# Optimization experiments

Hardware: AMD Instinct MI355X
Metric: run time of the kernel (lower is better)

The kernel has to match this reference:

```python
import jax, jax.numpy as jnp
import numpy as np

B, C, H, W = 8, 320, 32, 32
HEADS, DHEAD = 8, 40
CTX_LEN, CTX_DIM = 77, 768
FF_INNER = 4 * C
GROUPS = 32
HW = H * W


def setup_inputs() -> dict:
    key = jax.random.key(0)
    ks = jax.random.split(key, 16)
    def nrm(k, shape, s=0.02):
        return (jax.random.normal(k, shape) * s).astype(jnp.float32)
    z = lambda *s: jnp.zeros(s, jnp.float32)
    o = lambda *s: jnp.ones(s, jnp.float32)
    inp = {}
    inp["x"] = jax.random.normal(ks[0], (B, C, H, W), jnp.float32)
    inp["context"] = jax.random.normal(ks[1], (B, CTX_LEN, CTX_DIM), jnp.float32)
    inp["vis_mask"] = jax.random.uniform(ks[2], (B, HW, HW)) > 0.5
    inp["v2t_mask"] = jax.random.uniform(ks[3], (B, HW, CTX_LEN)) > 0.5
    inp["gn_scale"] = o(C); inp["gn_bias"] = z(C)
    inp["proj_in_w"] = nrm(ks[4], (C, C)); inp["proj_in_b"] = z(C)
    inp["n1_s"] = o(C); inp["n1_b"] = z(C)
    inp["wq1"] = nrm(ks[5], (C, C)); inp["wk1"] = nrm(ks[6], (C, C)); inp["wv1"] = nrm(ks[7], (C, C))
    inp["wo1"] = nrm(ks[8], (C, C)); inp["bo1"] = z(C)
    inp["n2_s"] = o(C); inp["n2_b"] = z(C)
    inp["wq2"] = nrm(ks[9], (C, C)); inp["wk2"] = nrm(ks[10], (CTX_DIM, C)); inp["wv2"] = nrm(ks[11], (CTX_DIM, C))
    inp["wo2"] = nrm(ks[12], (C, C)); inp["bo2"] = z(C)
    inp["n3_s"] = o(C); inp["n3_b"] = z(C)
    inp["ff_w1"] = nrm(ks[13], (C, 2 * FF_INNER)); inp["ff_b1"] = z(2 * FF_INNER)
    inp["ff_w2"] = nrm(ks[14], (FF_INNER, C)); inp["ff_b2"] = z(C)
    inp["proj_out_w"] = nrm(ks[15], (C, C)); inp["proj_out_b"] = z(C)
    return inp


def group_norm(x, scale, bias, eps=1e-6):
    b, c, h, w = x.shape
    xg = x.reshape(b, GROUPS, -1)
    mu = xg.mean(-1, keepdims=True)
    var = xg.var(-1, keepdims=True)
    xn = ((xg - mu) * jax.lax.rsqrt(var + eps)).reshape(b, c, h, w)
    return xn * scale[None, :, None, None] + bias[None, :, None, None]


def layer_norm(x, s, b, eps=1e-5):
    mu = x.mean(-1, keepdims=True)
    var = x.var(-1, keepdims=True)
    return (x - mu) * jax.lax.rsqrt(var + eps) * s + b


def mha(xq, ctx, wq, wk, wv, wo, bo, mask):
    # CrossAttention: manual einsum softmax with boolean mask broadcast over heads
    b, n, _ = xq.shape
    m = ctx.shape[1]
    split = lambda t: t.reshape(b, -1, HEADS, DHEAD).transpose(0, 2, 1, 3)
    q = split(xq @ wq)   # [b,h,n,d]
    k = split(ctx @ wk)  # [b,h,m,d]
    v = split(ctx @ wv)
    sim = jnp.einsum('bhid,bhjd->bhij', q, k) * (DHEAD ** -0.5)
    if mask is not None:
        sim = jnp.where(mask[:, None, :, :], sim, jnp.finfo(sim.dtype).min)
    attn = jax.nn.softmax(sim, axis=-1)
    out = jnp.einsum('bhij,bhjd->bhid', attn, v)
    out = out.transpose(0, 2, 1, 3).reshape(b, n, HEADS * DHEAD)
    return out @ wo + bo


def reference(x, context, vis_mask, v2t_mask, gn_scale, gn_bias, proj_in_w, proj_in_b,
              n1_s, n1_b, wq1, wk1, wv1, wo1, bo1,
              n2_s, n2_b, wq2, wk2, wv2, wo2, bo2,
              n3_s, n3_b, ff_w1, ff_b1, ff_w2, ff_b2,
              proj_out_w, proj_out_b):
    x_in = x
    h = group_norm(x, gn_scale, gn_bias)
    # 1x1 conv proj_in == per-pixel linear; flatten b c h w -> b (hw) c
    h = h.reshape(B, C, HW).transpose(0, 2, 1) @ proj_in_w + proj_in_b
    # masked self-attention (vis mask)
    h = h + mha(layer_norm(h, n1_s, n1_b), layer_norm(h, n1_s, n1_b),
                wq1, wk1, wv1, wo1, bo1, vis_mask)
    # masked cross-attention to text (v2t mask)
    h = h + mha(layer_norm(h, n2_s, n2_b), context,
                wq2, wk2, wv2, wo2, bo2, v2t_mask)
    # GEGLU feedforward (glu=True, mult=4)
    y = layer_norm(h, n3_s, n3_b) @ ff_w1 + ff_b1
    a, g = jnp.split(y, 2, axis=-1)
    h = h + (a * jax.nn.gelu(g, approximate=False)) @ ff_w2 + ff_b2
    # proj_out + residual
    out = (h @ proj_out_w + proj_out_b).transpose(0, 2, 1).reshape(B, C, H, W)
    return out + x_in
```

## Files before the change

### kernel.cpp

```cpp
#include <hip/hip_runtime.h>
#include <hip/hip_bf16.h>
#include <math.h>


#define Bsz   8
#define Cch   320
#define HW    1024
#define NTOK  (Bsz*HW)
#define HEADS 8
#define DHEAD 40
#define CTXL  77
#define CTXD  768
#define FFI   1280
#define MCTX  (Bsz*CTXL)
#define MCTXP 640

typedef unsigned short u16;
typedef unsigned long long u64;
typedef __attribute__((ext_vector_type(8))) u16    u16x8;
typedef __attribute__((ext_vector_type(8))) __bf16 bf16x8;
typedef __attribute__((ext_vector_type(4))) float  f32x4;

__device__ inline u16 f2b(float f) {
    unsigned u = __float_as_uint(f);
    return (u16)((u + 0x7FFFu + ((u >> 16) & 1u)) >> 16);
}

__global__ __launch_bounds__(256) void gn_stats(
    const float* __restrict__ x, const float* __restrict__ scale,
    const float* __restrict__ bias, float* __restrict__ gnA,
    float* __restrict__ gnB)
{
    int blk = blockIdx.x;
    int b = blk >> 5, g = blk & 31;
    int tid = threadIdx.x;
    __shared__ float rs[256], rq[256];
    const float4* xg = (const float4*)(x + ((size_t)b*Cch + g*10)*HW);
    float s = 0.f, q = 0.f;
    #pragma unroll
    for (int i = 0; i < 10; ++i) {
        float4 v = xg[tid + i*256];
        s += v.x + v.y + v.z + v.w;
        q += v.x*v.x + v.y*v.y + v.z*v.z + v.w*v.w;
    }
    rs[tid] = s; rq[tid] = q; __syncthreads();
    for (int off = 128; off > 0; off >>= 1) {
        if (tid < off) { rs[tid] += rs[tid+off]; rq[tid] += rq[tid+off]; }
        __syncthreads();
    }
    if (tid < 10) {
        float mean = rs[0] * (1.f/10240.f);
        float var  = rq[0] * (1.f/10240.f) - mean*mean;
        float inv  = rsqrtf(var + 1e-6f);
        int ch = g*10 + tid;
        float a = inv * scale[ch];
        gnA[b*Cch + ch] = a;
        gnB[b*Cch + ch] = bias[ch] - mean*a;
    }
}

__global__ __launch_bounds__(256) void gn_apply(
    const float* __restrict__ x, const float* __restrict__ gnA,
    const float* __restrict__ gnB, u16* __restrict__ out)
{
    __shared__ u16 T[64*72];
    const int tid = threadIdx.x;
    const int c0 = blockIdx.x * 64;
    const int p0 = blockIdx.y * 64;
    const int b  = blockIdx.z;
    for (int e = tid; e < 512; e += 256) {
        int r = e >> 3, ch = e & 7;
        const float* src = x + ((size_t)(b*Cch + c0 + r))*HW + p0 + ch*8;
        float a  = gnA[b*Cch + c0 + r];
        float bb = gnB[b*Cch + c0 + r];
        float4 v0 = *(const float4*)src;
        float4 v1 = *(const float4*)(src + 4);
        u16x8 val;
        val[0] = f2b(v0.x*a + bb); val[1] = f2b(v0.y*a + bb);
        val[2] = f2b(v0.z*a + bb); val[3] = f2b(v0.w*a + bb);
        val[4] = f2b(v1.x*a + bb); val[5] = f2b(v1.y*a + bb);
        val[6] = f2b(v1.z*a + bb); val[7] = f2b(v1.w*a + bb);
// ... 26 lines not shown
        sum += __shfl_xor(sum, off);
        sq  += __shfl_xor(sq,  off);
    }
    float mean = sum * (1.f/320.f);
    float var  = sq  * (1.f/320.f) - mean*mean;
    float inv  = rsqrtf(var + 1e-5f);
    u16* orow = out + (size_t)t*Cch;
    #pragma unroll
    for (int i = 0; i < 5; ++i) {
        int c = lane + 64*i;
        orow[c] = f2b((v[i]-mean)*inv*s[c] + bgain[c]);
    }
}

struct WDesc { const float* src; u16* dst; int K; int N; int tiles; float scl; };
struct WPack { WDesc w[12]; };

#define WT_TILES 620
#define CTXBLK   240

__global__ __launch_bounds__(256) void preamble(
    WPack p, const float* __restrict__ ctxsrc, u16* __restrict__ ctxdst,
    const void* __restrict__ vis, const void* __restrict__ v2t,
    u64* __restrict__ bvis, u64* __restrict__ bv2t)
{
    __shared__ u16 T[64*72];
    int blk = blockIdx.x;
    int tid = threadIdx.x;
    if (blk < WT_TILES) {
        int t = blk;
        #pragma unroll
        for (int i = 0; i < 12; ++i) {
            int nt = p.w[i].tiles;
            if (t < nt) {
                const int K = p.w[i].K, N = p.w[i].N;
                const int ntN = N >> 6;
                const int tk = t / ntN, tn = t - tk*ntN;
                const float scl = p.w[i].scl;
                const float* src = p.w[i].src;
                u16* dst = p.w[i].dst;
                for (int e = tid; e < 512; e += 256) {
                    int r = e >> 3, ch = e & 7;
                    const float* sp = src + (size_t)(tk*64 + r)*N + tn*64 + ch*8;
                    float4 v0 = *(const float4*)sp;
                    float4 v1 = *(const float4*)(sp + 4);
                    u16x8 val;
                    val[0] = f2b(v0.x*scl); val[1] = f2b(v0.y*scl);
// ... 9 lines not shown
                    dst[(size_t)(tn*64 + n)*K + tk*64 + k] = v;
                }
                return;
            }
            t -= nt;
        }
        return;
    }
    if (blk < WT_TILES + CTXBLK) {
        int idx = (blk - WT_TILES)*2048 + tid*8;
        int r = idx / CTXD;
        u16x8 val = {};
        if (r < MCTX) {
            float4 v0 = *(const float4*)(ctxsrc + idx);
            float4 v1 = *(const float4*)(ctxsrc + idx + 4);
            val[0] = f2b(v0.x); val[1] = f2b(v0.y);
            val[2] = f2b(v0.z); val[3] = f2b(v0.w);
            val[4] = f2b(v1.x); val[5] = f2b(v1.y);
            val[6] = f2b(v1.z); val[7] = f2b(v1.w);
        }
        *(u16x8*)(ctxdst + idx) = val;
        return;
    }
    __shared__ int any;
    if (tid == 0) any = 0;
    __syncthreads();
    const unsigned char* probe = (const unsigned char*)vis;
    for (int i = tid; i < 4096; i += 256)
        if ((i & 3) && probe[i]) any = 1;
    __syncthreads();
    const int isU8 = any;
    int mb = blk - WT_TILES - CTXBLK;
    const void* mask; u64* bits; int Lkv, nw;
    if (mb < 2048) { mask = vis; bits = bvis; Lkv = HW;   nw = 16; }
    else           { mask = v2t; bits = bv2t; Lkv = CTXL; nw = 2; mb -= 2048; }
    const int wv = tid >> 6, lane = tid & 63;
    const int row = mb*4 + wv;
    const unsigned char* m8  = (const unsigned char*)mask;
    const int*           m32 = (const int*)mask;
    const size_t base = (size_t)row * Lkv;
    for (int w = 0; w < nw; ++w) {
        int j = w*64 + lane;
        bool on = (j < Lkv) && (isU8 ? (m8[base+j] != 0) : (m32[base+j] != 0));
        u64 word = __ballot(on);
        if (lane == 0) bits[(size_t)row*nw + w] = word;
    }
}

__global__ __launch_bounds__(256) void gemm_bf16(
    const u16* __restrict__ A, const u16* __restrict__ Wt,
    const float* __restrict__ bias, const float* __restrict__ res,
    float* __restrict__ out, u16* __restrict__ out_bf, int M, int N, int K)
{
    __shared__ u16 As[2][128*40];
    __shared__ u16 Bs[2][64*40];
    const int tid  = threadIdx.x;
    const int lane = tid & 63;
    const int w    = tid >> 6;
    const int m0   = blockIdx.y * 128;
    const int n0   = blockIdx.x * 64;
    const int fr   = lane & 15, fg = lane >> 4;
    const int ar   = tid >> 2, ac = tid & 3;

    const u16* pa0 = A  + (size_t)(m0 + ar)*K      + ac*8;
    const u16* pa1 = A  + (size_t)(m0 + ar + 64)*K + ac*8;
    const u16* pb  = Wt + (size_t)(n0 + ar)*K      + ac*8;
    const int nk = K >> 5;

    *(u16x8*)&As[0][ar*40 + ac*8]      = *(const u16x8*)pa0;
    *(u16x8*)&As[0][(ar+64)*40 + ac*8] = *(const u16x8*)pa1;
    *(u16x8*)&Bs[0][ar*40 + ac*8]      = *(const u16x8*)pb;
    u16x8 xa0 = *(const u16x8*)(pa0 + 32);
    u16x8 xa1 = *(const u16x8*)(pa1 + 32);
    u16x8 xb  = *(const u16x8*)(pb  + 32);
    u16x8 ya0 = *(const u16x8*)(pa0 + 64);
    u16x8 ya1 = *(const u16x8*)(pa1 + 64);
    u16x8 yb  = *(const u16x8*)(pb  + 64);

    f32x4 acc[2][4] = {};
    for (int i = 0; i < nk; i += 2) {
        __syncthreads();
        *(u16x8*)&As[1][ar*40 + ac*8]      = xa0;
        *(u16x8*)&As[1][(ar+64)*40 + ac*8] = xa1;
        *(u16x8*)&Bs[1][ar*40 + ac*8]      = xb;
        if (i + 3 < nk) {
            xa0 = *(const u16x8*)(pa0 + 32*(i+3));
            xa1 = *(const u16x8*)(pa1 + 32*(i+3));
            xb  = *(const u16x8*)(pb  + 32*(i+3));
        }
        {
            bf16x8 a0 = *(const bf16x8*)&As[0][(w*32      + fr)*40 + fg*8];
            bf16x8 a1 = *(const bf16x8*)&As[0][(w*32 + 16 + fr)*40 + fg*8];
            #pragma unroll
            for (int nt = 0; nt < 4; ++nt) {
                bf16x8 b = *(const bf16x8*)&Bs[0][(nt*16 + fr)*40 + fg*8];
                acc[0][nt] = __builtin_amdgcn_mfma_f32_16x16x32_bf16(a0, b, acc[0][nt], 0, 0, 0);
                acc[1][nt] = __builtin_amdgcn_mfma_f32_16x16x32_bf16(a1, b, acc[1][nt], 0, 0, 0);
            }
        }
        __syncthreads();
        if (i + 2 < nk) {
            *(u16x8*)&As[0][ar*40 + ac*8]      = ya0;
            *(u16x8*)&As[0][(ar+64)*40 + ac*8] = ya1;
            *(u16x8*)&Bs[0][ar*40 + ac*8]      = yb;
            if (i + 4 < nk) {
                ya0 = *(const u16x8*)(pa0 + 32*(i+4));
                ya1 = *(const u16x8*)(pa1 + 32*(i+4));
                yb  = *(const u16x8*)(pb  + 32*(i+4));
            }
        }
        {
            bf16x8 a0 = *(const bf16x8*)&As[1][(w*32      + fr)*40 + fg*8];
            bf16x8 a1 = *(const bf16x8*)&As[1][(w*32 + 16 + fr)*40 + fg*8];
            #pragma unroll
            for (int nt = 0; nt < 4; ++nt) {
                bf16x8 b = *(const bf16x8*)&Bs[1][(nt*16 + fr)*40 + fg*8];
                acc[0][nt] = __builtin_amdgcn_mfma_f32_16x16x32_bf16(a0, b, acc[0][nt], 0, 0, 0);
                acc[1][nt] = __builtin_amdgcn_mfma_f32_16x16x32_bf16(a1, b, acc[1][nt], 0, 0, 0);
            }
        }
    }
    #pragma unroll
    for (int at = 0; at < 2; ++at) {
        #pragma unroll
        for (int nt = 0; nt < 4; ++nt) {
            int gn = n0 + nt*16 + fr;
            float bv = bias ? bias[gn] : 0.f;
            #pragma unroll
            for (int i = 0; i < 4; ++i) {
                int gm = m0 + w*32 + at*16 + fg*4 + i;
                float v = acc[at][nt][i] + bv;
                if (res) v += res[(size_t)gm*N + gn];
                if (out) out[(size_t)gm*N + gn] = v;
                if (out_bf) out_bf[(size_t)gm*N + gn] = f2b(v);
            }
        }
    }
}

__global__ __launch_bounds__(256) void gemm_pout(
    const u16* __restrict__ A, const u16* __restrict__ Wt,
    const float* __restrict__ bias, const float* __restrict__ x,
    float* __restrict__ out, int K)
{
    __shared__ u16 As[2][128*40];
    __shared__ u16 Bs[2][64*40];
    const int tid  = threadIdx.x;
    const int lane = tid & 63;
    const int w    = tid >> 6;
    const int m0   = blockIdx.y * 128;
    const int n0   = blockIdx.x * 64;
    const int fr   = lane & 15, fg = lane >> 4;
    const int ar   = tid >> 2, ac = tid & 3;

    const u16* pa0 = A  + (size_t)(m0 + ar)*K      + ac*8;
    const u16* pa1 = A  + (size_t)(m0 + ar + 64)*K + ac*8;
    const u16* pb  = Wt + (size_t)(n0 + ar)*K      + ac*8;
    const int nk = K >> 5;

    *(u16x8*)&As[0][ar*40 + ac*8]      = *(const u16x8*)pa0;
    *(u16x8*)&As[0][(ar+64)*40 + ac*8] = *(const u16x8*)pa1;
    *(u16x8*)&Bs[0][ar*40 + ac*8]      = *(const u16x8*)pb;
    u16x8 xa0 = *(const u16x8*)(pa0 + 32);
    u16x8 xa1 = *(const u16x8*)(pa1 + 32);
    u16x8 xb  = *(const u16x8*)(pb  + 32);
    u16x8 ya0 = *(const u16x8*)(pa0 + 64);
    u16x8 ya1 = *(const u16x8*)(pa1 + 64);
    u16x8 yb  = *(const u16x8*)(pb  + 64);

    f32x4 acc[2][4] = {};
    for (int i = 0; i < nk; i += 2) {
        __syncthreads();
        *(u16x8*)&As[1][ar*40 + ac*8]      = xa0;
        *(u16x8*)&As[1][(ar+64)*40 + ac*8] = xa1;
        *(u16x8*)&Bs[1][ar*40 + ac*8]      = xb;
        if (i + 3 < nk) {
            xa0 = *(const u16x8*)(pa0 + 32*(i+3));
            xa1 = *(const u16x8*)(pa1 + 32*(i+3));
            xb  = *(const u16x8*)(pb  + 32*(i+3));
        }
        {
            bf16x8 a0 = *(const bf16x8*)&As[0][(w*32      + fr)*40 + fg*8];
            bf16x8 a1 = *(const bf16x8*)&As[0][(w*32 + 16 + fr)*40 + fg*8];
            #pragma unroll
            for (int nt = 0; nt < 4; ++nt) {
                bf16x8 b = *(const bf16x8*)&Bs[0][(nt*16 + fr)*40 + fg*8];
                acc[0][nt] = __builtin_amdgcn_mfma_f32_16x16x32_bf16(a0, b, acc[0][nt], 0, 0, 0);
                acc[1][nt] = __builtin_amdgcn_mfma_f32_16x16x32_bf16(a1, b, acc[1][nt], 0, 0, 0);
            }
        }
        __syncthreads();
        if (i + 2 < nk) {
            *(u16x8*)&As[0][ar*40 + ac*8]      = ya0;
            *(u16x8*)&As[0][(ar+64)*40 + ac*8] = ya1;
            *(u16x8*)&Bs[0][ar*40 + ac*8]      = yb;
            if (i + 4 < nk) {
                ya0 = *(const u16x8*)(pa0 + 32*(i+4));
                ya1 = *(const u16x8*)(pa1 + 32*(i+4));
                yb  = *(const u16x8*)(pb  + 32*(i+4));
            }
        }
        {
            bf16x8 a0 = *(const bf16x8*)&As[1][(w*32      + fr)*40 + fg*8];
            bf16x8 a1 = *(const bf16x8*)&As[1][(w*32 + 16 + fr)*40 + fg*8];
            #pragma unroll
            for (int nt = 0; nt < 4; ++nt) {
                bf16x8 b = *(const bf16x8*)&Bs[1][(nt*16 + fr)*40 + fg*8];
                acc[0][nt] = __builtin_amdgcn_mfma_f32_16x16x32_bf16(a0, b, acc[0][nt], 0, 0, 0);
                acc[1][nt] = __builtin_amdgcn_mfma_f32_16x16x32_bf16(a1, b, acc[1][nt], 0, 0, 0);
            }
        }
    }
    #pragma unroll
    for (int at = 0; at < 2; ++at) {
        #pragma unroll
        for (int nt = 0; nt < 4; ++nt) {
            int gn = n0 + nt*16 + fr;
            float bv = bias[gn];
            int gm0 = m0 + w*32 + at*16 + fg*4;
            int b   = gm0 >> 10;
            int p   = gm0 & (HW-1);
            size_t o = ((size_t)(b*Cch + gn))*HW + p;
            f32x4 xv = *(const f32x4*)&x[o];
            f32x4 vv;
            #pragma unroll
            for (int i = 0; i < 4; ++i) vv[i] = acc[at][nt][i] + bv + xv[i];
            *(f32x4*)&out[o] = vv;
        }
    }
}

__global__ __launch_bounds__(256) void ctx_kv_gemm(
    const u16* __restrict__ ctx, const u16* __restrict__ wk,
    const u16* __restrict__ wv, u16* __restrict__ kout, u16* __restrict__ vout)
{
    __shared__ u16 As[2][64*40];
    __shared__ u16 Bs[2][64*40];
    const int tid  = threadIdx.x;
    const int lane = tid & 63;
    const int w    = tid >> 6;
    const int m0   = blockIdx.y * 64;
    const int n0   = blockIdx.x * 64;
    const u16* Wt  = blockIdx.z ? wv : wk;
    u16* outp      = blockIdx.z ? vout : kout;
    const int fr   = lane & 15, fg = lane >> 4;
    const int ar   = tid >> 2, ac = tid & 3;

    const u16* pa = ctx + (size_t)(m0 + ar)*CTXD + ac*8;
    const u16* pb = Wt  + (size_t)(n0 + ar)*CTXD + ac*8;
    const int nk = CTXD >> 5;

    *(u16x8*)&As[0][ar*40 + ac*8] = *(const u16x8*)pa;
    *(u16x8*)&Bs[0][ar*40 + ac*8] = *(const u16x8*)pb;
    u16x8 xa = *(const u16x8*)(pa + 32);
    u16x8 xb = *(const u16x8*)(pb + 32);
    u16x8 ya = *(const u16x8*)(pa + 64);
    u16x8 yb = *(const u16x8*)(pb + 64);

    f32x4 acc[4] = {};
    for (int i = 0; i < nk; i += 2) {
        __syncthreads();
        *(u16x8*)&As[1][ar*40 + ac*8] = xa;
        *(u16x8*)&Bs[1][ar*40 + ac*8] = xb;
        if (i + 3 < nk) {
            xa = *(const u16x8*)(pa + 32*(i+3));
            xb = *(const u16x8*)(pb + 32*(i+3));
        }
        {
            bf16x8 a = *(const bf16x8*)&As[0][(w*16 + fr)*40 + fg*8];
            #pragma unroll
            for (int nt = 0; nt < 4; ++nt) {
                bf16x8 b = *(const bf16x8*)&Bs[0][(nt*16 + fr)*40 + fg*8];
                acc[nt] = __builtin_amdgcn_mfma_f32_16x16x32_bf16(a, b, acc[nt], 0, 0, 0);
            }
        }
        __syncthreads();
        if (i + 2 < nk) {
            *(u16x8*)&As[0][ar*40 + ac*8] = ya;
            *(u16x8*)&Bs[0][ar*40 + ac*8] = yb;
            if (i + 4 < nk) {
                ya = *(const u16x8*)(pa + 32*(i+4));
                yb = *(const u16x8*)(pb + 32*(i+4));
            }
        }
        {
            bf16x8 a = *(const bf16x8*)&As[1][(w*16 + fr)*40 + fg*8];
            #pragma unroll
            for (int nt = 0; nt < 4; ++nt) {
                bf16x8 b = *(const bf16x8*)&Bs[1][(nt*16 + fr)*40 + fg*8];
                acc[nt] = __builtin_amdgcn_mfma_f32_16x16x32_bf16(a, b, acc[nt], 0, 0, 0);
            }
        }
    }
    #pragma unroll
    for (int nt = 0; nt < 4; ++nt) {
        int gn = n0 + nt*16 + fr;
        #pragma unroll
        for (int i = 0; i < 4; ++i) {
            int gm = m0 + w*16 + fg*4 + i;
            if (gm < MCTX)
                outp[(size_t)gm*Cch + gn] = f2b(acc[nt][i]);
        }
    }
}

__global__ __launch_bounds__(256) void geglu_bf16(
    const u16* __restrict__ A, const u16* __restrict__ Wt,
    const float* __restrict__ b1, u16* __restrict__ out, int M, int K)
{
    __shared__ u16 As[2][128*40];
    __shared__ u16 Ba[2][64*40];
    __shared__ u16 Bg[2][64*40];
    const int tid  = threadIdx.x;
    const int lane = tid & 63;
    const int w    = tid >> 6;
    const int m0   = blockIdx.y * 128;
    const int n0   = blockIdx.x * 64;
    const int fr   = lane & 15, fg = lane >> 4;
    const int ar   = tid >> 2, ac = tid & 3;

    const u16* pa0 = A  + (size_t)(m0 + ar)*K      + ac*8;
    const u16* pa1 = A  + (size_t)(m0 + ar + 64)*K + ac*8;
    const u16* pba = Wt + (size_t)(n0 + ar)*K       + ac*8;
    const u16* pbg = Wt + (size_t)(FFI + n0 + ar)*K + ac*8;
// ... 124 lines not shown
    const int w    = tid >> 6;
    const int col  = lane & 15;
    const int quad = lane >> 4;
    const int q0   = blockIdx.x * 64;
    const int h    = blockIdx.y;
    const int b    = blockIdx.z;
    const int ch   = tid & 7;
    const int r0   = tid >> 3;

    {
        const u16* qT = qb + ((size_t)(b*HW + q0))*qstride + (size_t)h*DHEAD + ch*8;
        u16x8 v0 = {}, v1 = {};
        if (ch < 5) {
            v0 = *(const u16x8*)(qT + (size_t)r0*qstride);
            v1 = *(const u16x8*)(qT + (size_t)(r0+32)*qstride);
        }
        *(u16x8*)&QPs[r0*72 + ch*8]      = v0;
        *(u16x8*)&QPs[(r0+32)*72 + ch*8] = v1;
    }
    __syncthreads();
    const bf16x8 qa0 = *(const bf16x8*)&QPs[(w*16 + col)*72 +  0 + quad*8];
    const bf16x8 qa1 = *(const bf16x8*)&QPs[(w*16 + col)*72 + 32 + quad*8];

    const u16* kT = kb + (size_t)b*Lkv*kstride + (size_t)h*DHEAD + ch*8;
    const bool kok = ch < 5;
    const u16* vT = vt + ((size_t)(b*Cch + h*DHEAD))*vstride + ch*8;
    const u64* mrow = mbits + ((size_t)(b*HW + q0 + w*16 + quad*4))*nw;

    f32x4 acc_o[3] = {};

    const int nkt = (Lkv + 63) / 64;
    for (int jt = 0; jt < nkt; ++jt) {
        const int j0 = jt*64;
        __syncthreads();
        {
            u16x8 v0 = {}, v1 = {};
            if (kok) {
                if (j0 + r0      < Lkv) v0 = *(const u16x8*)(kT + (size_t)(j0 + r0)*kstride);
                if (j0 + r0 + 32 < Lkv) v1 = *(const u16x8*)(kT + (size_t)(j0 + r0 + 32)*kstride);
            }
            *(u16x8*)&Ks[r0*72 + ch*8]      = v0;
            *(u16x8*)&Ks[(r0+32)*72 + ch*8] = v1;
        }
        {
            u16x8 v0 = {};
            if (r0 < DHEAD) v0 = *(const u16x8*)(vT + (size_t)r0*vstride + j0);
            *(u16x8*)&Vs[r0*72 + ch*8] = v0;
            if (tid < 128) {
                int d1 = 32 + (tid >> 3);
                u16x8 v1 = {};
                if (d1 < DHEAD) v1 = *(const u16x8*)(vT + (size_t)d1*vstride + j0);
                else if (d1 == DHEAD) {
                    #pragma unroll
                    for (int z = 0; z < 8; ++z) v1[z] = 0x3F80;
                }
                *(u16x8*)&Vs[d1*72 + ch*8] = v1;
            }
        }
        __syncthreads();

        u64 mw[4];
        #pragma unroll
        for (int i = 0; i < 4; ++i) mw[i] = mrow[i*nw + jt];

        f32x4 s[4] = {};
        #pragma unroll
        for (int nt = 0; nt < 4; ++nt) {
            bf16x8 b0 = *(const bf16x8*)&Ks[(nt*16 + col)*72 +  0 + quad*8];
            bf16x8 b1 = *(const bf16x8*)&Ks[(nt*16 + col)*72 + 32 + quad*8];
            s[nt] = __builtin_amdgcn_mfma_f32_16x16x32_bf16(qa0, b0, s[nt], 0, 0, 0);
            s[nt] = __builtin_amdgcn_mfma_f32_16x16x32_bf16(qa1, b1, s[nt], 0, 0, 0);
        }

        #pragma unroll
        for (int i = 0; i < 4; ++i) {
            #pragma unroll
            for (int nt = 0; nt < 4; ++nt) {
                float p = __expf(s[nt][i]);
                unsigned bits = (unsigned)(mw[i] >> (nt*16));
                s[nt][i] = ((bits >> col) & 1u) ? p : 0.f;
            }
        }

        #pragma unroll
        for (int nt = 0; nt < 4; ++nt)
            #pragma unroll
            for (int i = 0; i < 4; ++i)
                QPs[(w*16 + quad*4 + i)*68 + nt*16 + col] =
                    (u16)(__float_as_uint(s[nt][i]) >> 16);

        bf16x8 pa0, pa1;
        __builtin_memcpy(&pa0, &QPs[(w*16 + col)*68 +  0 + quad*8], 16);
        __builtin_memcpy(&pa1, &QPs[(w*16 + col)*68 + 32 + quad*8], 16);
        #pragma unroll
        for (int nt = 0; nt < 3; ++nt) {
            bf16x8 vb0 = *(const bf16x8*)&Vs[(nt*16 + col)*72 +  0 + quad*8];
            bf16x8 vb1 = *(const bf16x8*)&Vs[(nt*16 + col)*72 + 32 + quad*8];
            acc_o[nt] = __builtin_amdgcn_mfma_f32_16x16x32_bf16(pa0, vb0, acc_o[nt], 0, 0, 0);
            acc_o[nt] = __builtin_amdgcn_mfma_f32_16x16x32_bf16(pa1, vb1, acc_o[nt], 0, 0, 0);
        }
    }

    float inv_l[4];
    #pragma unroll
    for (int i = 0; i < 4; ++i)
        inv_l[i] = 1.f / __shfl(acc_o[2][i], (lane & 48) | 8);

    #pragma unroll
    for (int nt = 0; nt < 3; ++nt) {
        int d = nt*16 + col;
        if (d < DHEAD) {
            #pragma unroll
            for (int i = 0; i < 4; ++i) {
                int q = q0 + w*16 + quad*4 + i;
                out[((size_t)(b*HW + q))*Cch + h*DHEAD + d] = f2b(acc_o[nt][i] * inv_l[i]);
            }
        }
    }
}

extern "C" void kernel_launch(void* const* d_in, const int* in_sizes, int n_in,
                              void* d_out, int out_size, void* d_ws, size_t ws_size,
                              hipStream_t stream)
// ... 41 lines not shown
    u16*   Hb_bf= T1b + TOKC;
    u16*   Wbf  = Hb_bf + TOKC;
    u64*   mb_vis = (u64*)(Wbf + 2539520);
    u64*   mb_v2t = mb_vis + 131072;
    u16*   ctx_bf = (u16*)(mb_v2t + 16384);
    u16*   Kc_bf  = ctx_bf + MCTXP*CTXD;
    u16*   Vc_bf  = Kc_bf + 640*Cch;
    float* gnA    = (float*)(Vc_bf + 640*Cch);
    float* gnB    = gnA + Bsz*Cch;

    u16* w_q1  = Wbf;
    u16* w_k1  = Wbf +  102400;
    u16* w_v1  = Wbf +  204800;
    u16* w_pin = Wbf +  307200;
    u16* w_o1  = Wbf +  409600;
    u16* w_q2  = Wbf +  512000;
    u16* w_o2  = Wbf +  614400;
    u16* w_ff1 = Wbf +  716800;
    u16* w_ff2 = Wbf + 1536000;
    u16* w_po  = Wbf + 1945600;
    u16* w_k2  = Wbf + 2048000;
    u16* w_v2  = Wbf + 2293760;

    const float scale = 0.15811388300841897f;
    WPack pack;
    pack.w[0]  = { wq1,       w_q1,  Cch, Cch, 25,  scale };
    pack.w[1]  = { wk1,       w_k1,  Cch, Cch, 25,  1.f };
    pack.w[2]  = { wv1,       w_v1,  Cch, Cch, 25,  1.f };
    pack.w[3]  = { proj_in_w, w_pin, Cch, Cch, 25,  1.f };
    pack.w[4]  = { wo1,       w_o1,  Cch, Cch, 25,  1.f };
    pack.w[5]  = { wq2,       w_q2,  Cch, Cch, 25,  scale };
    pack.w[6]  = { wo2,       w_o2,  Cch, Cch, 25,  1.f };
    pack.w[7]  = { ff_w1,     w_ff1, Cch, 2*FFI, 200, 1.f };
    pack.w[8]  = { ff_w2,     w_ff2, FFI, Cch, 100, 1.f };
    pack.w[9]  = { pout_w,    w_po,  Cch, Cch, 25,  1.f };
    pack.w[10] = { wk2,       w_k2,  CTXD, Cch, 60, 1.f };
    pack.w[11] = { wv2,       w_v2,  CTXD, Cch, 60, 1.f };

    dim3 blk256(256);
    dim3 gTok(Cch/64, NTOK/128);
    dim3 gQKV(960/64, NTOK/128);
    dim3 gKV(Cch/64, MCTXP/64, 2);
    dim3 gFF(FFI/64, NTOK/128);
    dim3 gFA(HW/64, HEADS, Bsz);
    dim3 gTrS(Cch/64, HW/64, Bsz);
    dim3 gTrX(Cch/64, 2, Bsz);
    dim3 gGN(Cch/64, HW/64, Bsz);

    preamble<<<WT_TILES + CTXBLK + 4096, blk256, 0, stream>>>(
        pack, context, ctx_bf, vis_mask, v2t_mask, mb_vis, mb_v2t);

    gn_stats<<<Bsz*32, blk256, 0, stream>>>(x, gn_s, gn_b, gnA, gnB);
    gn_apply<<<gGN, blk256, 0, stream>>>(x, gnA, gnB, T0b);
    gemm_bf16<<<gTok, blk256, 0, stream>>>(T0b, w_pin, proj_in_b, nullptr, Hb, nullptr, NTOK, Cch, Cch);

    layernorm_kernel<<<NTOK/4, blk256, 0, stream>>>(Hb, n1_s, n1_b, T0b);
    gemm_bf16<<<gQKV, blk256, 0, stream>>>(T0b, w_q1, nullptr, nullptr, nullptr, QKV, NTOK, 960, Cch);
    transpose_v<<<gTrS, blk256, 0, stream>>>(QKV + 640, 960, Vt_g, HW, HW);
    flash_mfma<<<gFA, blk256, 0, stream>>>(QKV, 960, QKV + 320, 960, Vt_g, HW,
                                           mb_vis, 16, T1b, HW);
    gemm_bf16<<<gTok, blk256, 0, stream>>>(T1b, w_o1, bo1, Hb, Hb, nullptr, NTOK, Cch, Cch);

    layernorm_kernel<<<NTOK/4, blk256, 0, stream>>>(Hb, n2_s, n2_b, T0b);
    gemm_bf16<<<gTok, blk256, 0, stream>>>(T0b, w_q2, nullptr, nullptr, nullptr, QKV, NTOK, Cch, Cch);
    ctx_kv_gemm<<<gKV, blk256, 0, stream>>>(ctx_bf, w_k2, w_v2, Kc_bf, Vc_bf);
    transpose_v<<<gTrX, blk256, 0, stream>>>(Vc_bf, Cch, Vt_g, CTXL, 128);
    flash_mfma<<<gFA, blk256, 0, stream>>>(QKV, Cch, Kc_bf, Cch, Vt_g, 128,
                                           mb_v2t, 2, T1b, CTXL);
    gemm_bf16<<<gTok, blk256, 0, stream>>>(T1b, w_o2, bo2, Hb, Hb, nullptr, NTOK, Cch, Cch);

    layernorm_kernel<<<NTOK/4, blk256, 0, stream>>>(Hb, n3_s, n3_b, T0b);
    geglu_bf16<<<gFF, blk256, 0, stream>>>(T0b, w_ff1, ff_b1, G_bf, NTOK, Cch);
    gemm_bf16<<<gTok, blk256, 0, stream>>>(G_bf, w_ff2, ff_b2, Hb, nullptr, Hb_bf, NTOK, Cch, FFI);

    gemm_pout<<<gTok, blk256, 0, stream>>>(Hb_bf, w_po, pout_b, x, out, Cch);
}
```

Measured before the change: 403.5 us.

## Use 512-thread GEMM blocks, fold GN stats into preamble, exp2 softmax

The bf16 GEMM, proj_out GEMM and context KV GEMM kernels now run 8 waves per block instead of 4. Each wave covers a 32x32 (or 16x32) sub-tile, so there are more waves in flight to hide latency, but each wave does less MFMA work per LDS load. The group-norm statistics kernel is merged into the preamble launch to save one kernel launch. The flash attention kernel now uses exp2 with log2(e) folded into the Q weight scale, and steps precomputed K/V row pointers instead of recomputing addresses each iteration.

```diff
diff --git a/kernel.cpp b/kernel.cpp
--- a/kernel.cpp
+++ b/kernel.cpp
@@ -24,39 +24,6 @@
 __device__ inline u16 f2b(float f) {
     unsigned u = __float_as_uint(f);
     return (u16)((u + 0x7FFFu + ((u >> 16) & 1u)) >> 16);
-}
-
-__global__ __launch_bounds__(256) void gn_stats(
-    const float* __restrict__ x, const float* __restrict__ scale,
-    const float* __restrict__ bias, float* __restrict__ gnA,
-    float* __restrict__ gnB)
-{
-    int blk = blockIdx.x;
-    int b = blk >> 5, g = blk & 31;
-    int tid = threadIdx.x;
-    __shared__ float rs[256], rq[256];
-    const float4* xg = (const float4*)(x + ((size_t)b*Cch + g*10)*HW);
-    float s = 0.f, q = 0.f;
-    #pragma unroll
-    for (int i = 0; i < 10; ++i) {
-        float4 v = xg[tid + i*256];
-        s += v.x + v.y + v.z + v.w;
-        q += v.x*v.x + v.y*v.y + v.z*v.z + v.w*v.w;
-    }
-    rs[tid] = s; rq[tid] = q; __syncthreads();
-    for (int off = 128; off > 0; off >>= 1) {
-        if (tid < off) { rs[tid] += rs[tid+off]; rq[tid] += rq[tid+off]; }
-        __syncthreads();
-    }
-    if (tid < 10) {
-        float mean = rs[0] * (1.f/10240.f);
-        float var  = rq[0] * (1.f/10240.f) - mean*mean;
-        float inv  = rsqrtf(var + 1e-6f);
-        int ch = g*10 + tid;
-        float a = inv * scale[ch];
-        gnA[b*Cch + ch] = a;
-        gnB[b*Cch + ch] = bias[ch] - mean*a;
-    }
 }
 
 __global__ __launch_bounds__(256) void gn_apply(
@@ -129,7 +96,10 @@
 __global__ __launch_bounds__(256) void preamble(
     WPack p, const float* __restrict__ ctxsrc, u16* __restrict__ ctxdst,
     const void* __restrict__ vis, const void* __restrict__ v2t,
-    u64* __restrict__ bvis, u64* __restrict__ bv2t)
+    u64* __restrict__ bvis, u64* __restrict__ bv2t,
+    const float* __restrict__ x, const float* __restrict__ gscale,
+    const float* __restrict__ gbias, float* __restrict__ gnA,
+    float* __restrict__ gnB)
 {
     __shared__ u16 T[64*72];
     int blk = blockIdx.x;
@@ -185,6 +155,34 @@
         *(u16x8*)(ctxdst + idx) = val;
         return;
     }
+    if (blk >= WT_TILES + CTXBLK + 4096) {
+        int gb = blk - (WT_TILES + CTXBLK + 4096);
+        int b = gb >> 5, g = gb & 31;
+        __shared__ float rs[256], rq[256];
+        const float4* xg = (const float4*)(x + ((size_t)b*Cch + g*10)*HW);
+        float s = 0.f, q = 0.f;
+        #pragma unroll
+        for (int i = 0; i < 10; ++i) {
+            float4 v = xg[tid + i*256];
+            s += v.x + v.y + v.z + v.w;
+            q += v.x*v.x + v.y*v.y + v.z*v.z + v.w*v.w;
+        }
+        rs[tid] = s; rq[tid] = q; __syncthreads();
+        for (int off = 128; off > 0; off >>= 1) {
+            if (tid < off) { rs[tid] += rs[tid+off]; rq[tid] += rq[tid+off]; }
+            __syncthreads();
+        }
+        if (tid < 10) {
+            float mean = rs[0] * (1.f/10240.f);
+            float var  = rq[0] * (1.f/10240.f) - mean*mean;
+            float inv  = rsqrtf(var + 1e-6f);
+            int chn = g*10 + tid;
+            float a = inv * gscale[chn];
+            gnA[b*Cch + chn] = a;
+            gnB[b*Cch + chn] = gbias[chn] - mean*a;
+        }
+        return;
+    }
     __shared__ int any;
     if (tid == 0) any = 0;
     __syncthreads();
@@ -210,7 +208,7 @@
     }
 }
 
-__global__ __launch_bounds__(256) void gemm_bf16(
+__global__ __launch_bounds__(512) void gemm_bf16(
     const u16* __restrict__ A, const u16* __restrict__ Wt,
     const float* __restrict__ bias, const float* __restrict__ res,
     float* __restrict__ out, u16* __restrict__ out_bf, int M, int N, int K)
@@ -220,79 +218,74 @@
     const int tid  = threadIdx.x;
     const int lane = tid & 63;
     const int w    = tid >> 6;
+    const int mp   = w >> 1;
+    const int np   = w & 1;
     const int m0   = blockIdx.y * 128;
     const int n0   = blockIdx.x * 64;
     const int fr   = lane & 15, fg = lane >> 4;
     const int ar   = tid >> 2, ac = tid & 3;
-
-    const u16* pa0 = A  + (size_t)(m0 + ar)*K      + ac*8;
-    const u16* pa1 = A  + (size_t)(m0 + ar + 64)*K + ac*8;
-    const u16* pb  = Wt + (size_t)(n0 + ar)*K      + ac*8;
+    const bool hasB = tid < 256;
+
+    const u16* pa = A  + (size_t)(m0 + ar)*K + ac*8;
+    const u16* pb = Wt + (size_t)(n0 + ar)*K + ac*8;
     const int nk = K >> 5;
 
-    *(u16x8*)&As[0][ar*40 + ac*8]      = *(const u16x8*)pa0;
-    *(u16x8*)&As[0][(ar+64)*40 + ac*8] = *(const u16x8*)pa1;
-    *(u16x8*)&Bs[0][ar*40 + ac*8]      = *(const u16x8*)pb;
-    u16x8 xa0 = *(const u16x8*)(pa0 + 32);
-    u16x8 xa1 = *(const u16x8*)(pa1 + 32);
-    u16x8 xb  = *(const u16x8*)(pb  + 32);
-    u16x8 ya0 = *(const u16x8*)(pa0 + 64);
-    u16x8 ya1 = *(const u16x8*)(pa1 + 64);
-    u16x8 yb  = *(const u16x8*)(pb  + 64);
-
-    f32x4 acc[2][4] = {};
+    *(u16x8*)&As[0][ar*40 + ac*8] = *(const u16x8*)pa;
+    if (hasB) *(u16x8*)&Bs[0][ar*40 + ac*8] = *(const u16x8*)pb;
+    u16x8 xa = *(const u16x8*)(pa + 32);
+    u16x8 ya = *(const u16x8*)(pa + 64);
+    u16x8 xb = {}, yb = {};
+    if (hasB) { xb = *(const u16x8*)(pb + 32); yb = *(const u16x8*)(pb + 64); }
+
+    f32x4 acc[2][2] = {};
     for (int i = 0; i < nk; i += 2) {
         __syncthreads();
-        *(u16x8*)&As[1][ar*40 + ac*8]      = xa0;
-        *(u16x8*)&As[1][(ar+64)*40 + ac*8] = xa1;
-        *(u16x8*)&Bs[1][ar*40 + ac*8]      = xb;
+        *(u16x8*)&As[1][ar*40 + ac*8] = xa;
+        if (hasB) *(u16x8*)&Bs[1][ar*40 + ac*8] = xb;
         if (i + 3 < nk) {
-            xa0 = *(const u16x8*)(pa0 + 32*(i+3));
-            xa1 = *(const u16x8*)(pa1 + 32*(i+3));
-            xb  = *(const u16x8*)(pb  + 32*(i+3));
-        }
-        {
-            bf16x8 a0 = *(const bf16x8*)&As[0][(w*32      + fr)*40 + fg*8];
-            bf16x8 a1 = *(const bf16x8*)&As[0][(w*32 + 16 + fr)*40 + fg*8];
-            #pragma unroll
-            for (int nt = 0; nt < 4; ++nt) {
-                bf16x8 b = *(const bf16x8*)&Bs[0][(nt*16 + fr)*40 + fg*8];
-                acc[0][nt] = __builtin_amdgcn_mfma_f32_16x16x32_bf16(a0, b, acc[0][nt], 0, 0, 0);
-                acc[1][nt] = __builtin_amdgcn_mfma_f32_16x16x32_bf16(a1, b, acc[1][nt], 0, 0, 0);
+            xa = *(const u16x8*)(pa + 32*(i+3));
+            if (hasB) xb = *(const u16x8*)(pb + 32*(i+3));
+        }
+        {
+            bf16x8 a0 = *(const bf16x8*)&As[0][(mp*32      + fr)*40 + fg*8];
+            bf16x8 a1 = *(const bf16x8*)&As[0][(mp*32 + 16 + fr)*40 + fg*8];
+            #pragma unroll
+            for (int t = 0; t < 2; ++t) {
+                bf16x8 b = *(const bf16x8*)&Bs[0][((np*2+t)*16 + fr)*40 + fg*8];
+                acc[0][t] = __builtin_amdgcn_mfma_f32_16x16x32_bf16(a0, b, acc[0][t], 0, 0, 0);
+                acc[1][t] = __builtin_amdgcn_mfma_f32_16x16x32_bf16(a1, b, acc[1][t], 0, 0, 0);
             }
         }
         __syncthreads();
         if (i + 2 < nk) {
-            *(u16x8*)&As[0][ar*40 + ac*8]      = ya0;
-            *(u16x8*)&As[0][(ar+64)*40 + ac*8] = ya1;
-            *(u16x8*)&Bs[0][ar*40 + ac*8]      = yb;
+            *(u16x8*)&As[0][ar*40 + ac*8] = ya;
+            if (hasB) *(u16x8*)&Bs[0][ar*40 + ac*8] = yb;
             if (i + 4 < nk) {
-                ya0 = *(const u16x8*)(pa0 + 32*(i+4));
-                ya1 = *(const u16x8*)(pa1 + 32*(i+4));
-                yb  = *(const u16x8*)(pb  + 32*(i+4));
-            }
-        }
-        {
-            bf16x8 a0 = *(const bf16x8*)&As[1][(w*32      + fr)*40 + fg*8];
-            bf16x8 a1 = *(const bf16x8*)&As[1][(w*32 + 16 + fr)*40 + fg*8];
-            #pragma unroll
-            for (int nt = 0; nt < 4; ++nt) {
-                bf16x8 b = *(const bf16x8*)&Bs[1][(nt*16 + fr)*40 + fg*8];
-                acc[0][nt] = __builtin_amdgcn_mfma_f32_16x16x32_bf16(a0, b, acc[0][nt], 0, 0, 0);
-                acc[1][nt] = __builtin_amdgcn_mfma_f32_16x16x32_bf16(a1, b, acc[1][nt], 0, 0, 0);
+                ya = *(const u16x8*)(pa + 32*(i+4));
+                if (hasB) yb = *(const u16x8*)(pb + 32*(i+4));
+            }
+        }
+        {
+            bf16x8 a0 = *(const bf16x8*)&As[1][(mp*32      + fr)*40 + fg*8];
+            bf16x8 a1 = *(const bf16x8*)&As[1][(mp*32 + 16 + fr)*40 + fg*8];
+            #pragma unroll
+            for (int t = 0; t < 2; ++t) {
+                bf16x8 b = *(const bf16x8*)&Bs[1][((np*2+t)*16 + fr)*40 + fg*8];
+                acc[0][t] = __builtin_amdgcn_mfma_f32_16x16x32_bf16(a0, b, acc[0][t], 0, 0, 0);
+                acc[1][t] = __builtin_amdgcn_mfma_f32_16x16x32_bf16(a1, b, acc[1][t], 0, 0, 0);
             }
         }
     }
     #pragma unroll
     for (int at = 0; at < 2; ++at) {
         #pragma unroll
-        for (int nt = 0; nt < 4; ++nt) {
-            int gn = n0 + nt*16 + fr;
+        for (int t = 0; t < 2; ++t) {
+            int gn = n0 + (np*2+t)*16 + fr;
             float bv = bias ? bias[gn] : 0.f;
             #pragma unroll
             for (int i = 0; i < 4; ++i) {
-                int gm = m0 + w*32 + at*16 + fg*4 + i;
-                float v = acc[at][nt][i] + bv;
+                int gm = m0 + mp*32 + at*16 + fg*4 + i;
+                float v = acc[at][t][i] + bv;
                 if (res) v += res[(size_t)gm*N + gn];
                 if (out) out[(size_t)gm*N + gn] = v;
                 if (out_bf) out_bf[(size_t)gm*N + gn] = f2b(v);
@@ -301,7 +294,7 @@
     }
 }
 
-__global__ __launch_bounds__(256) void gemm_pout(
+__global__ __launch_bounds__(512) void gemm_pout(
     const u16* __restrict__ A, const u16* __restrict__ Wt,
     const float* __restrict__ bias, const float* __restrict__ x,
     float* __restrict__ out, int K)
@@ -311,89 +304,84 @@
     const int tid  = threadIdx.x;
     const int lane = tid & 63;
     const int w    = tid >> 6;
+    const int mp   = w >> 1;
+    const int np   = w & 1;
     const int m0   = blockIdx.y * 128;
     const int n0   = blockIdx.x * 64;
     const int fr   = lane & 15, fg = lane >> 4;
     const int ar   = tid >> 2, ac = tid & 3;
-
-    const u16* pa0 = A  + (size_t)(m0 + ar)*K      + ac*8;
-    const u16* pa1 = A  + (size_t)(m0 + ar + 64)*K + ac*8;
-    const u16* pb  = Wt + (size_t)(n0 + ar)*K      + ac*8;
+    const bool hasB = tid < 256;
+
+    const u16* pa = A  + (size_t)(m0 + ar)*K + ac*8;
+    const u16* pb = Wt + (size_t)(n0 + ar)*K + ac*8;
     const int nk = K >> 5;
 
-    *(u16x8*)&As[0][ar*40 + ac*8]      = *(const u16x8*)pa0;
-    *(u16x8*)&As[0][(ar+64)*40 + ac*8] = *(const u16x8*)pa1;
-    *(u16x8*)&Bs[0][ar*40 + ac*8]      = *(const u16x8*)pb;
-    u16x8 xa0 = *(const u16x8*)(pa0 + 32);
-    u16x8 xa1 = *(const u16x8*)(pa1 + 32);
-    u16x8 xb  = *(const u16x8*)(pb  + 32);
-    u16x8 ya0 = *(const u16x8*)(pa0 + 64);
-    u16x8 ya1 = *(const u16x8*)(pa1 + 64);
-    u16x8 yb  = *(const u16x8*)(pb  + 64);
-
-    f32x4 acc[2][4] = {};
+    *(u16x8*)&As[0][ar*40 + ac*8] = *(const u16x8*)pa;
+    if (hasB) *(u16x8*)&Bs[0][ar*40 + ac*8] = *(const u16x8*)pb;
+    u16x8 xa = *(const u16x8*)(pa + 32);
+    u16x8 ya = *(const u16x8*)(pa + 64);
+    u16x8 xb = {}, yb = {};
+    if (hasB) { xb = *(const u16x8*)(pb + 32); yb = *(const u16x8*)(pb + 64); }
+
+    f32x4 acc[2][2] = {};
     for (int i = 0; i < nk; i += 2) {
         __syncthreads();
-        *(u16x8*)&As[1][ar*40 + ac*8]      = xa0;
-        *(u16x8*)&As[1][(ar+64)*40 + ac*8] = xa1;
-        *(u16x8*)&Bs[1][ar*40 + ac*8]      = xb;
+        *(u16x8*)&As[1][ar*40 + ac*8] = xa;
+        if (hasB) *(u16x8*)&Bs[1][ar*40 + ac*8] = xb;
         if (i + 3 < nk) {
-            xa0 = *(const u16x8*)(pa0 + 32*(i+3));
-            xa1 = *(const u16x8*)(pa1 + 32*(i+3));
-            xb  = *(const u16x8*)(pb  + 32*(i+3));
-        }
-        {
-            bf16x8 a0 = *(const bf16x8*)&As[0][(w*32      + fr)*40 + fg*8];
-            bf16x8 a1 = *(const bf16x8*)&As[0][(w*32 + 16 + fr)*40 + fg*8];
-            #pragma unroll
-            for (int nt = 0; nt < 4; ++nt) {
-                bf16x8 b = *(const bf16x8*)&Bs[0][(nt*16 + fr)*40 + fg*8];
-                acc[0][nt] = __builtin_amdgcn_mfma_f32_16x16x32_bf16(a0, b, acc[0][nt], 0, 0, 0);
-                acc[1][nt] = __builtin_amdgcn_mfma_f32_16x16x32_bf16(a1, b, acc[1][nt], 0, 0, 0);
+            xa = *(const u16x8*)(pa + 32*(i+3));
+            if (hasB) xb = *(const u16x8*)(pb + 32*(i+3));
+        }
+        {
+            bf16x8 a0 = *(const bf16x8*)&As[0][(mp*32      + fr)*40 + fg*8];
+            bf16x8 a1 = *(const bf16x8*)&As[0][(mp*32 + 16 + fr)*40 + fg*8];
+            #pragma unroll
+            for (int t = 0; t < 2; ++t) {
+                bf16x8 b = *(const bf16x8*)&Bs[0][((np*2+t)*16 + fr)*40 + fg*8];
+                acc[0][t] = __builtin_amdgcn_mfma_f32_16x16x32_bf16(a0, b, acc[0][t], 0, 0, 0);
+                acc[1][t] = __builtin_amdgcn_mfma_f32_16x16x32_bf16(a1, b, acc[1][t], 0, 0, 0);
             }
         }
         __syncthreads();
         if (i + 2 < nk) {
-            *(u16x8*)&As[0][ar*40 + ac*8]      = ya0;
-            *(u16x8*)&As[0][(ar+64)*40 + ac*8] = ya1;
-            *(u16x8*)&Bs[0][ar*40 + ac*8]      = yb;
+            *(u16x8*)&As[0][ar*40 + ac*8] = ya;
+            if (hasB) *(u16x8*)&Bs[0][ar*40 + ac*8] = yb;
             if (i + 4 < nk) {
-                ya0 = *(const u16x8*)(pa0 + 32*(i+4));
-                ya1 = *(const u16x8*)(pa1 + 32*(i+4));
-                yb  = *(const u16x8*)(pb  + 32*(i+4));
-            }
-        }
-        {
-            bf16x8 a0 = *(const bf16x8*)&As[1][(w*32      + fr)*40 + fg*8];
-            bf16x8 a1 = *(const bf16x8*)&As[1][(w*32 + 16 + fr)*40 + fg*8];
-            #pragma unroll
-            for (int nt = 0; nt < 4; ++nt) {
-                bf16x8 b = *(const bf16x8*)&Bs[1][(nt*16 + fr)*40 + fg*8];
-                acc[0][nt] = __builtin_amdgcn_mfma_f32_16x16x32_bf16(a0, b, acc[0][nt], 0, 0, 0);
-                acc[1][nt] = __builtin_amdgcn_mfma_f32_16x16x32_bf16(a1, b, acc[1][nt], 0, 0, 0);
+                ya = *(const u16x8*)(pa + 32*(i+4));
+                if (hasB) yb = *(const u16x8*)(pb + 32*(i+4));
+            }
+        }
+        {
+            bf16x8 a0 = *(const bf16x8*)&As[1][(mp*32      + fr)*40 + fg*8];
+            bf16x8 a1 = *(const bf16x8*)&As[1][(mp*32 + 16 + fr)*40 + fg*8];
+            #pragma unroll
+            for (int t = 0; t < 2; ++t) {
+                bf16x8 b = *(const bf16x8*)&Bs[1][((np*2+t)*16 + fr)*40 + fg*8];
+                acc[0][t] = __builtin_amdgcn_mfma_f32_16x16x32_bf16(a0, b, acc[0][t], 0, 0, 0);
+                acc[1][t] = __builtin_amdgcn_mfma_f32_16x16x32_bf16(a1, b, acc[1][t], 0, 0, 0);
             }
         }
     }
     #pragma unroll
     for (int at = 0; at < 2; ++at) {
         #pragma unroll
-        for (int nt = 0; nt < 4; ++nt) {
-            int gn = n0 + nt*16 + fr;
+        for (int t = 0; t < 2; ++t) {
+            int gn = n0 + (np*2+t)*16 + fr;
             float bv = bias[gn];
-            int gm0 = m0 + w*32 + at*16 + fg*4;
+            int gm0 = m0 + mp*32 + at*16 + fg*4;
             int b   = gm0 >> 10;
-            int p   = gm0 & (HW-1);
-            size_t o = ((size_t)(b*Cch + gn))*HW + p;
+            int pcol= gm0 & (HW-1);
+            size_t o = ((size_t)(b*Cch + gn))*HW + pcol;
             f32x4 xv = *(const f32x4*)&x[o];
             f32x4 vv;
             #pragma unroll
-            for (int i = 0; i < 4; ++i) vv[i] = acc[at][nt][i] + bv + xv[i];
+            for (int i = 0; i < 4; ++i) vv[i] = acc[at][t][i] + bv + xv[i];
             *(f32x4*)&out[o] = vv;
         }
     }
 }
 
-__global__ __launch_bounds__(256) void ctx_kv_gemm(
+__global__ __launch_bounds__(512) void ctx_kv_gemm(
     const u16* __restrict__ ctx, const u16* __restrict__ wk,
     const u16* __restrict__ wv, u16* __restrict__ kout, u16* __restrict__ vout)
 {
@@ -402,67 +390,61 @@
     const int tid  = threadIdx.x;
     const int lane = tid & 63;
     const int w    = tid >> 6;
+    const int mg   = w >> 1;
+    const int np   = w & 1;
     const int m0   = blockIdx.y * 64;
     const int n0   = blockIdx.x * 64;
     const u16* Wt  = blockIdx.z ? wv : wk;
     u16* outp      = blockIdx.z ? vout : kout;
     const int fr   = lane & 15, fg = lane >> 4;
-    const int ar   = tid >> 2, ac = tid & 3;
-
-    const u16* pa = ctx + (size_t)(m0 + ar)*CTXD + ac*8;
-    const u16* pb = Wt  + (size_t)(n0 + ar)*CTXD + ac*8;
+    const bool isA = tid < 256;
+    const int cr   = (tid & 255) >> 2, cc = tid & 3;
+
+    const u16* ps = isA ? ctx + (size_t)(m0 + cr)*CTXD + cc*8
+                        : Wt  + (size_t)(n0 + cr)*CTXD + cc*8;
+    u16* s0 = isA ? &As[0][cr*40 + cc*8] : &Bs[0][cr*40 + cc*8];
+    u16* s1 = isA ? &As[1][cr*40 + cc*8] : &Bs[1][cr*40 + cc*8];
     const int nk = CTXD >> 5;
 
-    *(u16x8*)&As[0][ar*40 + ac*8] = *(const u16x8*)pa;
-    *(u16x8*)&Bs[0][ar*40 + ac*8] = *(const u16x8*)pb;
-    u16x8 xa = *(const u16x8*)(pa + 32);
-    u16x8 xb = *(const u16x8*)(pb + 32);
-    u16x8 ya = *(const u16x8*)(pa + 64);
-    u16x8 yb = *(const u16x8*)(pb + 64);
-
-    f32x4 acc[4] = {};
+    *(u16x8*)s0 = *(const u16x8*)ps;
+    u16x8 xv = *(const u16x8*)(ps + 32);
+    u16x8 yv = *(const u16x8*)(ps + 64);
+
+    f32x4 acc[2] = {};
     for (int i = 0; i < nk; i += 2) {
         __syncthreads();
-        *(u16x8*)&As[1][ar*40 + ac*8] = xa;
-        *(u16x8*)&Bs[1][ar*40 + ac*8] = xb;
-        if (i + 3 < nk) {
-            xa = *(const u16x8*)(pa + 32*(i+3));
-            xb = *(const u16x8*)(pb + 32*(i+3));
-        }
-        {
-            bf16x8 a = *(const bf16x8*)&As[0][(w*16 + fr)*40 + fg*8];
-            #pragma unroll
-            for (int nt = 0; nt < 4; ++nt) {
-                bf16x8 b = *(const bf16x8*)&Bs[0][(nt*16 + fr)*40 + fg*8];
-                acc[nt] = __builtin_amdgcn_mfma_f32_16x16x32_bf16(a, b, acc[nt], 0, 0, 0);
+        *(u16x8*)s1 = xv;
+        if (i + 3 < nk) xv = *(const u16x8*)(ps + 32*(i+3));
+        {
+            bf16x8 a = *(const bf16x8*)&As[0][(mg*16 + fr)*40 + fg*8];
+            #pragma unroll
+            for (int t = 0; t < 2; ++t) {
+                bf16x8 b = *(const bf16x8*)&Bs[0][((np*2+t)*16 + fr)*40 + fg*8];
+                acc[t] = __builtin_amdgcn_mfma_f32_16x16x32_bf16(a, b, acc[t], 0, 0, 0);
             }
         }
         __syncthreads();
         if (i + 2 < nk) {
-            *(u16x8*)&As[0][ar*40 + ac*8] = ya;
-            *(u16x8*)&Bs[0][ar*40 + ac*8] = yb;
-            if (i + 4 < nk) {
-                ya = *(const u16x8*)(pa + 32*(i+4));
-                yb = *(const u16x8*)(pb + 32*(i+4));
-            }
-        }
-        {
-            bf16x8 a = *(const bf16x8*)&As[1][(w*16 + fr)*40 + fg*8];
-            #pragma unroll
-            for (int nt = 0; nt < 4; ++nt) {
-                bf16x8 b = *(const bf16x8*)&Bs[1][(nt*16 + fr)*40 + fg*8];
-                acc[nt] = __builtin_amdgcn_mfma_f32_16x16x32_bf16(a, b, acc[nt], 0, 0, 0);
+            *(u16x8*)s0 = yv;
+            if (i + 4 < nk) yv = *(const u16x8*)(ps + 32*(i+4));
+        }
+        {
+            bf16x8 a = *(const bf16x8*)&As[1][(mg*16 + fr)*40 + fg*8];
+            #pragma unroll
+            for (int t = 0; t < 2; ++t) {
+                bf16x8 b = *(const bf16x8*)&Bs[1][((np*2+t)*16 + fr)*40 + fg*8];
+                acc[t] = __builtin_amdgcn_mfma_f32_16x16x32_bf16(a, b, acc[t], 0, 0, 0);
             }
         }
     }
     #pragma unroll
-    for (int nt = 0; nt < 4; ++nt) {
-        int gn = n0 + nt*16 + fr;
+    for (int t = 0; t < 2; ++t) {
+        int gn = n0 + (np*2+t)*16 + fr;
         #pragma unroll
         for (int i = 0; i < 4; ++i) {
-            int gm = m0 + w*16 + fg*4 + i;
+            int gm = m0 + mg*16 + fg*4 + i;
             if (gm < MCTX)
-                outp[(size_t)gm*Cch + gn] = f2b(acc[nt][i]);
+                outp[(size_t)gm*Cch + gn] = f2b(acc[t][i]);
         }
     }
 }
@@ -633,9 +615,15 @@
     const bf16x8 qa0 = *(const bf16x8*)&QPs[(w*16 + col)*72 +  0 + quad*8];
     const bf16x8 qa1 = *(const bf16x8*)&QPs[(w*16 + col)*72 + 32 + quad*8];
 
-    const u16* kT = kb + (size_t)b*Lkv*kstride + (size_t)h*DHEAD + ch*8;
     const bool kok = ch < 5;
-    const u16* vT = vt + ((size_t)(b*Cch + h*DHEAD))*vstride + ch*8;
+    const u16* kR0 = kb + (size_t)b*Lkv*kstride + (size_t)h*DHEAD + ch*8
+                        + (size_t)r0*kstride;
+    const u16* kR1 = kR0 + (size_t)32*kstride;
+    const int d1   = 32 + (tid >> 3);
+    const u16* vR0 = vt + ((size_t)(b*Cch + h*DHEAD))*vstride + ch*8
+                        + (size_t)r0*vstride;
+    const u16* vR1 = vt + ((size_t)(b*Cch + h*DHEAD))*vstride + ch*8
+                        + (size_t)d1*vstride;
     const u64* mrow = mbits + ((size_t)(b*HW + q0 + w*16 + quad*4))*nw;
 
     f32x4 acc_o[3] = {};
@@ -646,21 +634,18 @@
         __syncthreads();
         {
             u16x8 v0 = {}, v1 = {};
-            if (kok) {
-                if (j0 + r0      < Lkv) v0 = *(const u16x8*)(kT + (size_t)(j0 + r0)*kstride);
-                if (j0 + r0 + 32 < Lkv) v1 = *(const u16x8*)(kT + (size_t)(j0 + r0 + 32)*kstride);
-            }
+            if (kok && (j0 + r0      < Lkv)) v0 = *(const u16x8*)kR0;
+            if (kok && (j0 + r0 + 32 < Lkv)) v1 = *(const u16x8*)kR1;
             *(u16x8*)&Ks[r0*72 + ch*8]      = v0;
             *(u16x8*)&Ks[(r0+32)*72 + ch*8] = v1;
         }
         {
             u16x8 v0 = {};
-            if (r0 < DHEAD) v0 = *(const u16x8*)(vT + (size_t)r0*vstride + j0);
+            if (r0 < DHEAD) v0 = *(const u16x8*)vR0;
             *(u16x8*)&Vs[r0*72 + ch*8] = v0;
             if (tid < 128) {
-                int d1 = 32 + (tid >> 3);
                 u16x8 v1 = {};
-                if (d1 < DHEAD) v1 = *(const u16x8*)(vT + (size_t)d1*vstride + j0);
+                if (d1 < DHEAD) v1 = *(const u16x8*)vR1;
                 else if (d1 == DHEAD) {
                     #pragma unroll
                     for (int z = 0; z < 8; ++z) v1[z] = 0x3F80;
@@ -687,7 +672,7 @@
         for (int i = 0; i < 4; ++i) {
             #pragma unroll
             for (int nt = 0; nt < 4; ++nt) {
-                float p = __expf(s[nt][i]);
+                float p = __builtin_amdgcn_exp2f(s[nt][i]);
                 unsigned bits = (unsigned)(mw[i] >> (nt*16));
                 s[nt][i] = ((bits >> col) & 1u) ? p : 0.f;
             }
@@ -710,6 +695,11 @@
             acc_o[nt] = __builtin_amdgcn_mfma_f32_16x16x32_bf16(pa0, vb0, acc_o[nt], 0, 0, 0);
             acc_o[nt] = __builtin_amdgcn_mfma_f32_16x16x32_bf16(pa1, vb1, acc_o[nt], 0, 0, 0);
         }
+
+        kR0 += (size_t)64*kstride;
+        kR1 += (size_t)64*kstride;
+        vR0 += 64;
+        vR1 += 64;
     }
 
     float inv_l[4];
@@ -797,14 +787,14 @@
     u16* w_k2  = Wbf + 2048000;
     u16* w_v2  = Wbf + 2293760;
 
-    const float scale = 0.15811388300841897f;
+    const float qscale = 0.15811388300841897f * 1.4426950408889634f;
     WPack pack;
-    pack.w[0]  = { wq1,       w_q1,  Cch, Cch, 25,  scale };
+    pack.w[0]  = { wq1,       w_q1,  Cch, Cch, 25,  qscale };
     pack.w[1]  = { wk1,       w_k1,  Cch, Cch, 25,  1.f };
     pack.w[2]  = { wv1,       w_v1,  Cch, Cch, 25,  1.f };
     pack.w[3]  = { proj_in_w, w_pin, Cch, Cch, 25,  1.f };
     pack.w[4]  = { wo1,       w_o1,  Cch, Cch, 25,  1.f };
-    pack.w[5]  = { wq2,       w_q2,  Cch, Cch, 25,  scale };
+    pack.w[5]  = { wq2,       w_q2,  Cch, Cch, 25,  qscale };
     pack.w[6]  = { wo2,       w_o2,  Cch, Cch, 25,  1.f };
     pack.w[7]  = { ff_w1,     w_ff1, Cch, 2*FFI, 200, 1.f };
     pack.w[8]  = { ff_w2,     w_ff2, FFI, Cch, 100, 1.f };
@@ -813,6 +803,7 @@
     pack.w[11] = { wv2,       w_v2,  CTXD, Cch, 60, 1.f };
 
     dim3 blk256(256);
+    dim3 blk512(512);
     dim3 gTok(Cch/64, NTOK/128);
     dim3 gQKV(960/64, NTOK/128);
     dim3 gKV(Cch/64, MCTXP/64, 2);
@@ -822,31 +813,31 @@
     dim3 gTrX(Cch/64, 2, Bsz);
     dim3 gGN(Cch/64, HW/64, Bsz);
 
-    preamble<<<WT_TILES + CTXBLK + 4096, blk256, 0, stream>>>(
-        pack, context, ctx_bf, vis_mask, v2t_mask, mb_vis, mb_v2t);
-
-    gn_stats<<<Bsz*32, blk256, 0, stream>>>(x, gn_s, gn_b, gnA, gnB);
+    preamble<<<WT_TILES + CTXBLK + 4096 + 256, blk256, 0, stream>>>(
+        pack, context, ctx_bf, vis_mask, v2t_mask, mb_vis, mb_v2t,
+        x, gn_s, gn_b, gnA, gnB);
+
     gn_apply<<<gGN, blk256, 0, stream>>>(x, gnA, gnB, T0b);
-    gemm_bf16<<<gTok, blk256, 0, stream>>>(T0b, w_pin, proj_in_b, nullptr, Hb, nullptr, NTOK, Cch, Cch);
+    gemm_bf16<<<gTok, blk512, 0, stream>>>(T0b, w_pin, proj_in_b, nullptr, Hb, nullptr, NTOK, Cch, Cch);
 
     layernorm_kernel<<<NTOK/4, blk256, 0, stream>>>(Hb, n1_s, n1_b, T0b);
-    gemm_bf16<<<gQKV, blk256, 0, stream>>>(T0b, w_q1, nullptr, nullptr, nullptr, QKV, NTOK, 960, Cch);
+    gemm_bf16<<<gQKV, blk512, 0, stream>>>(T0b, w_q1, nullptr, nullptr, nullptr, QKV, NTOK, 960, Cch);
     transpose_v<<<gTrS, blk256, 0, stream>>>(QKV + 640, 960, Vt_g, HW, HW);
     flash_mfma<<<gFA, blk256, 0, stream>>>(QKV, 960, QKV + 320, 960, Vt_g, HW,
                                            mb_vis, 16, T1b, HW);
-    gemm_bf16<<<gTok, blk256, 0, stream>>>(T1b, w_o1, bo1, Hb, Hb, nullptr, NTOK, Cch, Cch);
+    gemm_bf16<<<gTok, blk512, 0, stream>>>(T1b, w_o1, bo1, Hb, Hb, nullptr, NTOK, Cch, Cch);
 
     layernorm_kernel<<<NTOK/4, blk256, 0, stream>>>(Hb, n2_s, n2_b, T0b);
-    gemm_bf16<<<gTok, blk256, 0, stream>>>(T0b, w_q2, nullptr, nullptr, nullptr, QKV, NTOK, Cch, Cch);
-    ctx_kv_gemm<<<gKV, blk256, 0, stream>>>(ctx_bf, w_k2, w_v2, Kc_bf, Vc_bf);
+    gemm_bf16<<<gTok, blk512, 0, stream>>>(T0b, w_q2, nullptr, nullptr, nullptr, QKV, NTOK, Cch, Cch);
+    ctx_kv_gemm<<<gKV, blk512, 0, stream>>>(ctx_bf, w_k2, w_v2, Kc_bf, Vc_bf);
     transpose_v<<<gTrX, blk256, 0, stream>>>(Vc_bf, Cch, Vt_g, CTXL, 128);
     flash_mfma<<<gFA, blk256, 0, stream>>>(QKV, Cch, Kc_bf, Cch, Vt_g, 128,
                                            mb_v2t, 2, T1b, CTXL);
-    gemm_bf16<<<gTok, blk256, 0, stream>>>(T1b, w_o2, bo2, Hb, Hb, nullptr, NTOK, Cch, Cch);
+    gemm_bf16<<<gTok, blk512, 0, stream>>>(T1b, w_o2, bo2, Hb, Hb, nullptr, NTOK, Cch, Cch);
 
     layernorm_kernel<<<NTOK/4, blk256, 0, stream>>>(Hb, n3_s, n3_b, T0b);
     geglu_bf16<<<gFF, blk256, 0, stream>>>(T0b, w_ff1, ff_b1, G_bf, NTOK, Cch);
-    gemm_bf16<<<gTok, blk256, 0, stream>>>(G_bf, w_ff2, ff_b2, Hb, nullptr, Hb_bf, NTOK, Cch, FFI);
-
-    gemm_pout<<<gTok, blk256, 0, stream>>>(Hb_bf, w_po, pout_b, x, out, Cch);
-}
+    gemm_bf16<<<gTok, blk512, 0, stream>>>(G_bf, w_ff2, ff_b2, Hb, nullptr, Hb_bf, NTOK, Cch, FFI);
+
+    gemm_pout<<<gTok, blk512, 0, stream>>>(Hb_bf, w_po, pout_b, x, out, Cch);
+}
```

New measurement: 387.9 us. 3.9% less time.
